# Kernel tuning notes

Measured on AMD Instinct MI355X. Metric: run time of the kernel, lower is better.

The kernel has to match this reference:

```python
import jax, jax.numpy as jnp
import numpy as np

B, S, D = 2, 2048, 2048
H, KV, HD = 32, 8, 64          # n_heads, n_kv_heads, head_dim
REP = H // KV                   # GQA repeat factor
NEG = -1e30                     # causal mask fill


def setup_inputs() -> dict:
    key = jax.random.key(0)
    ks = jax.random.split(key, 5)
    x = jax.random.normal(ks[0], (B, S, D), dtype=jnp.float32)
    # llama rotary frequencies: theta = 10000^{-2i/hd}
    inv_freq = 1.0 / (10000.0 ** (np.arange(0, HD, 2, dtype=np.float32) / HD))
    angles = np.outer(np.arange(S, dtype=np.float32), inv_freq)  # (S, HD/2)
    freqs_cos = jnp.asarray(np.cos(angles), dtype=jnp.float32)
    freqs_sin = jnp.asarray(np.sin(angles), dtype=jnp.float32)
    sc = 0.02
    wq = jax.random.normal(ks[1], (H * HD, D), dtype=jnp.float32) * sc
    wk = jax.random.normal(ks[2], (KV * HD, D), dtype=jnp.float32) * sc
    wv = jax.random.normal(ks[3], (KV * HD, D), dtype=jnp.float32) * sc
    wo = jax.random.normal(ks[4], (D, H * HD), dtype=jnp.float32) * sc
    return {"x": x, "freqs_cos": freqs_cos, "freqs_sin": freqs_sin,
            "wq": wq, "wk": wk, "wv": wv, "wo": wo}


def _rope(t, cos, sin):
    # t: (B, S, h, HD); even/odd lanes form (real, imag) pairs
    tr, ti = t[..., 0::2], t[..., 1::2]
    cos = cos[None, :, None, :]
    sin = sin[None, :, None, :]
    out_r = tr * cos - ti * sin
    out_i = tr * sin + ti * cos
    return jnp.stack([out_r, out_i], axis=-1).reshape(t.shape)


def reference(x, freqs_cos, freqs_sin, wq, wk, wv, wo):
    # QKV projections (torch Linear convention: y = x @ W.T)
    q = (x @ wq.T).reshape(B, S, H, HD)
    k = (x @ wk.T).reshape(B, S, KV, HD)
    v = (x @ wv.T).reshape(B, S, KV, HD)
    q = _rope(q, freqs_cos, freqs_sin)
    k = _rope(k, freqs_cos, freqs_sin)
    # GQA: group query heads instead of materializing repeat_kv
    q = q.transpose(0, 2, 1, 3).reshape(B, KV, REP, S, HD)  # (B,g,r,S,HD)
    k = k.transpose(0, 2, 1, 3)                              # (B,g,S,HD)
    v = v.transpose(0, 2, 1, 3)                              # (B,g,S,HD)
    scores = jnp.einsum('bgrqh,bgkh->bgrqk', q, k) / np.float32(np.sqrt(HD))
    causal = jnp.tril(jnp.ones((S, S), dtype=bool))
    scores = jnp.where(causal[None, None, None], scores, NEG)
    probs = jax.nn.softmax(scores, axis=-1)
    out = jnp.einsum('bgrqk,bgkh->bgrqh', probs, v)
    out = out.reshape(B, H, S, HD).transpose(0, 2, 1, 3).reshape(B, S, H * HD)
    return out @ wo.T
```

## Files before the change

kernel.cpp:

```cpp
#include <hip/hip_runtime.h>
#include <stdint.h>

#define S_LEN 2048
#define D_DIM 2048
#define NH 32
#define NKV 8
#define HD 64
#define B_SZ 2
#define QKV_N 3072
#define K_OFF 2048
#define V_OFF 2560
#define SCL 0.1803368801111244f

typedef unsigned short ushort_t;
typedef __attribute__((ext_vector_type(8))) short short8;
typedef __attribute__((ext_vector_type(4))) float f32x4;
typedef __attribute__((ext_vector_type(16))) float f32x16;

__device__ __forceinline__ float b2f(ushort_t u) {
  union { unsigned int i; float f; } x; x.i = ((unsigned int)u) << 16; return x.f;
}
__device__ __forceinline__ ushort_t f2b(float f) {
  union { float f; unsigned int i; } x; x.f = f;
  unsigned int r = x.i + 0x7FFFu + ((x.i >> 16) & 1u);
  return (ushort_t)(r >> 16);
}

__device__ __forceinline__ void load_lds16(const ushort_t* g, ushort_t* l) {
  __builtin_amdgcn_global_load_lds(
      (const __attribute__((address_space(1))) void*)g,
      (__attribute__((address_space(3))) void*)l, 16, 0, 0);
}

__device__ __forceinline__ short8 ld_swz(const ushort_t* base, int row, int colElem) {
  int byte = (row << 7) + (colElem << 1);
  byte ^= (row & 7) << 4;
  return *(const short8*)((const char*)base + byte);
}

__device__ __forceinline__ uint32_t cvtpk(float a, float b) {
  uint32_t r;
  asm("v_cvt_pk_bf16_f32 %0, %1, %2" : "=v"(r) : "v"(a), "v"(b));
  return r;
}
__device__ __forceinline__ void pswap(uint32_t& a, uint32_t& b) {
  asm("v_permlane32_swap_b32 %0, %1" : "+v"(a), "+v"(b));
}
__device__ __forceinline__ short8 mk8(uint32_t w0, uint32_t w1, uint32_t w2, uint32_t w3) {
  union { uint32_t w[4]; short8 v; } u;
  u.w[0] = w0; u.w[1] = w1; u.w[2] = w2; u.w[3] = w3;
  return u.v;
}

__global__ void cvt_bf16(const float* __restrict__ in, ushort_t* __restrict__ out, int n8) {
  int i = blockIdx.x * blockDim.x + threadIdx.x;
  if (i >= n8) return;
  const float4* p = (const float4*)(in + (size_t)i * 8);
  float4 x0 = p[0], x1 = p[1];
  ushort_t u[8] = { f2b(x0.x), f2b(x0.y), f2b(x0.z), f2b(x0.w),
                    f2b(x1.x), f2b(x1.y), f2b(x1.z), f2b(x1.w) };
  *(uint4*)(out + (size_t)i * 8) = *(const uint4*)u;
}

template <int HEADS, int LOG2H>
__global__ void rope_kernel(ushort_t* __restrict__ t, const float* __restrict__ cosT,
                            const float* __restrict__ sinT, int n8) {
  int idx = blockIdx.x * blockDim.x + threadIdx.x;
  if (idx >= n8) return;
  int d8 = idx & 7;
  int rest = idx >> 3;
  int h = rest & (HEADS - 1);
  int row = rest >> LOG2H;
  int s = row & (S_LEN - 1);
  float4 c4 = *(const float4*)(cosT + s * 32 + d8 * 4);
  float4 s4 = *(const float4*)(sinT + s * 32 + d8 * 4);
  ushort_t* p = t + (size_t)row * QKV_N + h * HD + d8 * 8;
  ushort_t u[8]; *(uint4*)u = *(const uint4*)p;
  float c[4] = { c4.x, c4.y, c4.z, c4.w }, sn[4] = { s4.x, s4.y, s4.z, s4.w };
  ushort_t o[8];
#pragma unroll
  for (int j = 0; j < 4; ++j) {
    float re = b2f(u[2 * j]), im = b2f(u[2 * j + 1]);
    o[2 * j]     = f2b(re * c[j] - im * sn[j]);
    o[2 * j + 1] = f2b(re * sn[j] + im * c[j]);
  }
  *(uint4*)p = *(const uint4*)o;
}

__global__ __launch_bounds__(256) void transpose_v(const ushort_t* __restrict__ v,
                                                   ushort_t* __restrict__ vt) {
  __shared__ ushort_t tile[64][80];
  int st = blockIdx.x, g = blockIdx.y, b = blockIdx.z;
  int tid = threadIdx.x;
#pragma unroll
  for (int p = 0; p < 2; ++p) {
    int o = p * 2048 + tid * 8;
    int s = o >> 6, d = o & 63;
    uint4 val = *(const uint4*)(v + ((size_t)(b * S_LEN + st * 64 + s) * QKV_N + g * HD + d));
    *(uint4*)&tile[s][d] = val;
  }
  __syncthreads();
#pragma unroll
  for (int p = 0; p < 2; ++p) {
    int o = p * 2048 + tid * 8;
    int d = o >> 6, s0 = o & 63;
    ushort_t tmp[8];
#pragma unroll
    for (int j = 0; j < 8; ++j) tmp[j] = tile[s0 + j][d];
    *(uint4*)(vt + (((size_t)(b * NKV + g) * HD + d) * S_LEN + st * 64 + s0)) = *(const uint4*)tmp;
  }
}

template <typename OutT>
__global__ __launch_bounds__(256) void gemm_bt(const ushort_t* __restrict__ A,
                                               const ushort_t* __restrict__ Bw,
                                               OutT* __restrict__ C,
                                               int M, int N, int K) {
  __shared__ ushort_t As[128 * 32];
  __shared__ ushort_t Bs[128 * 32];
  const int tid = threadIdx.x;
  const int lane = tid & 63, wave = tid >> 6;
  const int wr = wave >> 1, wc = wave & 1;
  const size_t rb = (size_t)blockIdx.y * 128;
  const size_t cb = (size_t)blockIdx.x * 128;
  f32x4 acc[4][4];
#pragma unroll
  for (int i = 0; i < 4; ++i)
#pragma unroll
    for (int j = 0; j < 4; ++j) acc[i][j] = (f32x4){0.f, 0.f, 0.f, 0.f};

  for (int k0 = 0; k0 < K; k0 += 32) {
    __syncthreads();
#pragma unroll
    for (int c = 0; c < 2; ++c) {
      const int o = c * 4096 + wave * 1024 + lane * 16;
      const int r = o >> 6;
      const int col = (o >> 1) & 31;
      load_lds16(A + (rb + r) * K + k0 + col, As + (c * 4096 + wave * 1024) / 2);
      load_lds16(Bw + (cb + r) * K + k0 + col, Bs + (c * 4096 + wave * 1024) / 2);
    }
    __syncthreads();
    short8 a[4], b[4];
#pragma unroll
    for (int i = 0; i < 4; ++i) {
      a[i] = *(const short8*)(As + (wr * 64 + i * 16 + (lane & 15)) * 32 + (lane >> 4) * 8);
      b[i] = *(const short8*)(Bs + (wc * 64 + i * 16 + (lane & 15)) * 32 + (lane >> 4) * 8);
    }
#pragma unroll
    for (int i = 0; i < 4; ++i)
#pragma unroll
      for (int j = 0; j < 4; ++j)
        acc[i][j] = __builtin_amdgcn_mfma_f32_16x16x32_bf16(a[i], b[j], acc[i][j], 0, 0, 0);
  }
#pragma unroll
  for (int i = 0; i < 4; ++i) {
    const size_t r0 = rb + wr * 64 + i * 16 + ((lane >> 4) * 4);
#pragma unroll
    for (int j = 0; j < 4; ++j) {
      const size_t c0 = cb + wc * 64 + j * 16 + (lane & 15);
#pragma unroll
      for (int r = 0; r < 4; ++r) {
        float v = acc[i][j][r];
        if constexpr (sizeof(OutT) == 2) C[(r0 + r) * N + c0] = f2b(v);
        else                             C[(r0 + r) * N + c0] = v;
      }
    }
  }
}

__global__ __launch_bounds__(256) void flash_attn(const ushort_t* __restrict__ q,
                                                  const ushort_t* __restrict__ k,
                                                  const ushort_t* __restrict__ vt,
                                                  ushort_t* __restrict__ out) {
  __shared__ ushort_t Ks[2][64 * 64];
  __shared__ ushort_t Vs[2][64 * 64];
  const int pairIdx = blockIdx.x, h = blockIdx.y, b = blockIdx.z;
  const int g = h >> 2;
  const int tid = threadIdx.x, lane = tid & 63, wave = tid >> 6;
  const int l31 = lane & 31, hi = lane >> 5;

  int srcRow[2], srcCol[2], ldsOff[2];
#pragma unroll
  for (int c = 0; c < 2; ++c) {
    const int o = c * 4096 + wave * 1024 + lane * 16;
    const int r = o >> 7;
    srcRow[c] = r;
    srcCol[c] = ((o & 127) ^ ((r & 7) << 4)) >> 1;
    ldsOff[c] = (c * 4096 + wave * 1024) / 2;
  }
  const ushort_t* kbase = k + (size_t)b * S_LEN * QKV_N + g * HD;
  const ushort_t* vbase = vt + (size_t)(b * NKV + g) * HD * S_LEN;

#pragma unroll 1
  for (int halfi = 0; halfi < 2; ++halfi) {
    const int qt = (halfi == 0) ? pairIdx : (15 - pairIdx);
    const int q0 = qt * 128;
    const int qwbase = q0 + wave * 32;
    const int qglob = qwbase + l31;

    short8 qf[4];
    {
      const ushort_t* qp = q + (size_t)(b * S_LEN + qglob) * QKV_N + h * HD + hi * 8;
#pragma unroll
      for (int s = 0; s < 4; ++s) qf[s] = *(const short8*)(qp + s * 16);
    }
    f32x16 oacc[2];
#pragma unroll
    for (int d = 0; d < 2; ++d)
#pragma unroll
      for (int r = 0; r < 16; ++r) oacc[d][r] = 0.f;
    float msc = -3e38f, lrow = 0.f;

#pragma unroll
    for (int c = 0; c < 2; ++c) {
      load_lds16(kbase + (size_t)srcRow[c] * QKV_N + srcCol[c], &Ks[0][ldsOff[c]]);
      load_lds16(vbase + (size_t)srcRow[c] * S_LEN + srcCol[c], &Vs[0][ldsOff[c]]);
    }
    __syncthreads();

    int cur = 0;
    const int nt = 2 * (qt + 1);
    for (int t = 0; t < nt; ++t) {
      const int kv0 = t * 64;
      if (t + 1 < nt) {
        const int nk = kv0 + 64;
#pragma unroll
        for (int c = 0; c < 2; ++c) {
          load_lds16(kbase + (size_t)(nk + srcRow[c]) * QKV_N + srcCol[c], &Ks[cur ^ 1][ldsOff[c]]);
          load_lds16(vbase + (size_t)srcRow[c] * S_LEN + nk + srcCol[c], &Vs[cur ^ 1][ldsOff[c]]);
        }
      }
      if (kv0 <= qwbase + 31) {
        f32x16 pacc[2];
#pragma unroll
        for (int j = 0; j < 2; ++j) {
          f32x16 z;
#pragma unroll
          for (int r = 0; r < 16; ++r) z[r] = 0.f;
#pragma unroll
          for (int s = 0; s < 4; ++s) {
            short8 kf = ld_swz(Ks[cur], j * 32 + l31, s * 16 + hi * 8);
            z = __builtin_amdgcn_mfma_f32_32x32x16_bf16(kf, qf[s], z, 0, 0, 0);
          }
          pacc[j] = z;
        }
        if (kv0 + 63 > qwbase) {
#pragma unroll
          for (int j = 0; j < 2; ++j)
#pragma unroll
            for (int r = 0; r < 16; ++r) {
              const int kvabs = kv0 + j * 32 + (r & 3) + 8 * (r >> 2) + 4 * hi;
              pacc[j][r] = (kvabs <= qglob) ? pacc[j][r] : -1e30f;
            }
        }
        float mraw = -3e38f;
#pragma unroll
        for (int j = 0; j < 2; ++j)
#pragma unroll
          for (int r = 0; r < 16; ++r) mraw = fmaxf(mraw, pacc[j][r]);
        mraw = fmaxf(mraw, __shfl_xor(mraw, 32));
        const float mscn = fmaxf(msc, mraw * SCL);
        const float sold = exp2f(msc - mscn);
        msc = mscn;
        float rs = 0.f;
        short8 pf[4];
#pragma unroll
        for (int j = 0; j < 2; ++j) {
          float pv[16];
#pragma unroll
          for (int r = 0; r < 16; ++r) {
            pv[r] = exp2f(pacc[j][r] * SCL - msc);
            rs += pv[r];
          }
          uint32_t w0 = cvtpk(pv[0], pv[1]),  w1 = cvtpk(pv[2], pv[3]);
          uint32_t w2 = cvtpk(pv[4], pv[5]),  w3 = cvtpk(pv[6], pv[7]);
          uint32_t w4 = cvtpk(pv[8], pv[9]),  w5 = cvtpk(pv[10], pv[11]);
          uint32_t w6 = cvtpk(pv[12], pv[13]), w7 = cvtpk(pv[14], pv[15]);
          pswap(w0, w2); pswap(w1, w3); pswap(w4, w6); pswap(w5, w7);
          pf[2 * j]     = mk8(w0, w1, w2, w3);
          pf[2 * j + 1] = mk8(w4, w5, w6, w7);
        }
        rs += __shfl_xor(rs, 32);
        lrow = lrow * sold + rs;
#pragma unroll
        for (int dblk = 0; dblk < 2; ++dblk) {
#pragma unroll
          for (int r = 0; r < 16; ++r) oacc[dblk][r] *= sold;
#pragma unroll
          for (int s = 0; s < 4; ++s) {
            short8 vf = ld_swz(Vs[cur], dblk * 32 + l31, s * 16 + hi * 8);
            oacc[dblk] = __builtin_amdgcn_mfma_f32_32x32x16_bf16(vf, pf[s], oacc[dblk], 0, 0, 0);
          }
        }
      }
      __syncthreads();
      cur ^= 1;
    }
    const float inv = 1.f / lrow;
    ushort_t* op = out + (size_t)(b * S_LEN + qglob) * (NH * HD) + h * HD;
#pragma unroll
    for (int dblk = 0; dblk < 2; ++dblk) {
      float ov[16];
#pragma unroll
      for (int r = 0; r < 16; ++r) ov[r] = oacc[dblk][r] * inv;
      uint32_t w0 = cvtpk(ov[0], ov[1]),  w1 = cvtpk(ov[2], ov[3]);
      uint32_t w2 = cvtpk(ov[4], ov[5]),  w3 = cvtpk(ov[6], ov[7]);
      uint32_t w4 = cvtpk(ov[8], ov[9]),  w5 = cvtpk(ov[10], ov[11]);
      uint32_t w6 = cvtpk(ov[12], ov[13]), w7 = cvtpk(ov[14], ov[15]);
      pswap(w0, w2); pswap(w1, w3); pswap(w4, w6); pswap(w5, w7);
      uint4 stlo; stlo.x = w0; stlo.y = w1; stlo.z = w2; stlo.w = w3;
      uint4 sthi; sthi.x = w4; sthi.y = w5; sthi.z = w6; sthi.w = w7;
      *(uint4*)(op + dblk * 32 + hi * 8)      = stlo;
      *(uint4*)(op + dblk * 32 + 16 + hi * 8) = sthi;
    }
  }
}

extern "C" void kernel_launch(void* const* d_in, const int* in_sizes, int n_in,
                              void* d_out, int out_size, void* d_ws, size_t ws_size,
                              hipStream_t stream) {
  const float* x  = (const float*)d_in[0];
  const float* fc = (const float*)d_in[1];
  const float* fs = (const float*)d_in[2];
  const float* wq = (const float*)d_in[3];
  const float* wk = (const float*)d_in[4];
  const float* wv = (const float*)d_in[5];
  const float* wo = (const float*)d_in[6];
  float* out = (float*)d_out;
  ushort_t* ws = (ushort_t*)d_ws;

  const size_t n_x   = (size_t)B_SZ * S_LEN * D_DIM;
  const size_t n_wq  = (size_t)NH * HD * D_DIM;
  const size_t n_wk  = (size_t)NKV * HD * D_DIM;
  const size_t n_qkv = (size_t)B_SZ * S_LEN * QKV_N;
  const size_t n_q   = (size_t)B_SZ * S_LEN * NH * HD;
  const size_t n_k   = (size_t)B_SZ * S_LEN * NKV * HD;

  size_t off = 0;
  ushort_t* xb   = ws + off; off += n_x;
  ushort_t* wqb  = ws + off; off += n_wq;
  ushort_t* wkb  = ws + off; off += n_wk;
  ushort_t* wvb  = ws + off; off += n_wk;
  ushort_t* wob  = ws + off; off += n_wq;
  ushort_t* qkvb = ws + off; off += n_qkv;
  ushort_t* vtb  = ws + off; off += n_k;
  ushort_t* ab   = ws + off; off += n_q;
  (void)ws_size; (void)in_sizes; (void)n_in; (void)out_size;

  auto cvt = [&](const float* src, ushort_t* dst, size_t n) {
    int n8 = (int)(n / 8);
    cvt_bf16<<<dim3((n8 + 255) / 256), dim3(256), 0, stream>>>(src, dst, n8);
  };
  cvt(x, xb, n_x);
  cvt(wq, wqb, n_wq);
  cvt(wk, wkb, n_wk);
  cvt(wv, wvb, n_wk);
  cvt(wo, wob, n_wq);

  const int M = B_SZ * S_LEN;
  gemm_bt<ushort_t><<<dim3(QKV_N / 128, M / 128), 256, 0, stream>>>(xb, wqb, qkvb, M, QKV_N, D_DIM);

  rope_kernel<NH, 5><<<dim3((M * NH * 8) / 256), 256, 0, stream>>>(qkvb, fc, fs, M * NH * 8);
  rope_kernel<NKV, 3><<<dim3((M * NKV * 8) / 256), 256, 0, stream>>>(qkvb + K_OFF, fc, fs, M * NKV * 8);

  transpose_v<<<dim3(S_LEN / 64, NKV, B_SZ), 256, 0, stream>>>(qkvb + V_OFF, vtb);

  flash_attn<<<dim3(8, NH, B_SZ), 256, 0, stream>>>(qkvb, qkvb + K_OFF, vtb, ab);

  gemm_bt<float><<<dim3(D_DIM / 128, M / 128), 256, 0, stream>>>(ab, wob, out, M, D_DIM, D_DIM);
}
```

Measured before the change: 244.3 us.

## Split flash-attention pairs into heaviest-first blocks, lazy rescale, XCD remap GEMM

Flash attention no longer pairs a light and a heavy query tile per block. It launches one block per query tile, ordered heaviest first, doubling the grid for better load balance across CUs. It also adds s_setprio around the MFMA sections and skips the running-max rescale unless the max grows by more than 8 (log2 units), which avoids exp and multiply work but lets unnormalised values grow. The GEMM block index is remapped so neighbouring tiles land on the same XCD, to improve L2 reuse.

```diff
diff --git a/kernel.cpp b/kernel.cpp
--- a/kernel.cpp
+++ b/kernel.cpp
@@ -121,8 +121,11 @@
   const int tid = threadIdx.x;
   const int lane = tid & 63, wave = tid >> 6;
   const int wr = wave >> 1, wc = wave & 1;
-  const size_t rb = (size_t)blockIdx.y * 128;
-  const size_t cb = (size_t)blockIdx.x * 128;
+  const int nwg = gridDim.x * gridDim.y;
+  const int orig = blockIdx.y * gridDim.x + blockIdx.x;
+  const int w = ((orig & 7) * (nwg >> 3)) + (orig >> 3);
+  const size_t rb = (size_t)(w / gridDim.x) * 128;
+  const size_t cb = (size_t)(w % gridDim.x) * 128;
   f32x4 acc[4][4];
 #pragma unroll
   for (int i = 0; i < 4; ++i)
@@ -174,7 +177,8 @@
                                                   ushort_t* __restrict__ out) {
   __shared__ ushort_t Ks[2][64 * 64];
   __shared__ ushort_t Vs[2][64 * 64];
-  const int pairIdx = blockIdx.x, h = blockIdx.y, b = blockIdx.z;
+  const int qt = 15 - blockIdx.x;
+  const int h = blockIdx.y, b = blockIdx.z;
   const int g = h >> 2;
   const int tid = threadIdx.x, lane = tid & 63, wave = tid >> 6;
   const int l31 = lane & 31, hi = lane >> 5;
@@ -191,128 +195,133 @@
   const ushort_t* kbase = k + (size_t)b * S_LEN * QKV_N + g * HD;
   const ushort_t* vbase = vt + (size_t)(b * NKV + g) * HD * S_LEN;
 
-#pragma unroll 1
-  for (int halfi = 0; halfi < 2; ++halfi) {
-    const int qt = (halfi == 0) ? pairIdx : (15 - pairIdx);
-    const int q0 = qt * 128;
-    const int qwbase = q0 + wave * 32;
-    const int qglob = qwbase + l31;
-
-    short8 qf[4];
-    {
-      const ushort_t* qp = q + (size_t)(b * S_LEN + qglob) * QKV_N + h * HD + hi * 8;
-#pragma unroll
-      for (int s = 0; s < 4; ++s) qf[s] = *(const short8*)(qp + s * 16);
-    }
-    f32x16 oacc[2];
-#pragma unroll
-    for (int d = 0; d < 2; ++d)
-#pragma unroll
-      for (int r = 0; r < 16; ++r) oacc[d][r] = 0.f;
-    float msc = -3e38f, lrow = 0.f;
-
-#pragma unroll
-    for (int c = 0; c < 2; ++c) {
-      load_lds16(kbase + (size_t)srcRow[c] * QKV_N + srcCol[c], &Ks[0][ldsOff[c]]);
-      load_lds16(vbase + (size_t)srcRow[c] * S_LEN + srcCol[c], &Vs[0][ldsOff[c]]);
+  const int qwbase = qt * 128 + wave * 32;
+  const int qglob = qwbase + l31;
+
+  short8 qf[4];
+  {
+    const ushort_t* qp = q + (size_t)(b * S_LEN + qglob) * QKV_N + h * HD + hi * 8;
+#pragma unroll
+    for (int s = 0; s < 4; ++s) qf[s] = *(const short8*)(qp + s * 16);
+  }
+  f32x16 oacc[2];
+#pragma unroll
+  for (int d = 0; d < 2; ++d)
+#pragma unroll
+    for (int r = 0; r < 16; ++r) oacc[d][r] = 0.f;
+  float msc = -3e38f, lrow = 0.f;
+
+#pragma unroll
+  for (int c = 0; c < 2; ++c) {
+    load_lds16(kbase + (size_t)srcRow[c] * QKV_N + srcCol[c], &Ks[0][ldsOff[c]]);
+    load_lds16(vbase + (size_t)srcRow[c] * S_LEN + srcCol[c], &Vs[0][ldsOff[c]]);
+  }
+  __syncthreads();
+
+  int cur = 0;
+  const int nt = 2 * (qt + 1);
+  for (int t = 0; t < nt; ++t) {
+    const int kv0 = t * 64;
+    if (t + 1 < nt) {
+      const int nk = kv0 + 64;
+#pragma unroll
+      for (int c = 0; c < 2; ++c) {
+        load_lds16(kbase + (size_t)(nk + srcRow[c]) * QKV_N + srcCol[c], &Ks[cur ^ 1][ldsOff[c]]);
+        load_lds16(vbase + (size_t)srcRow[c] * S_LEN + nk + srcCol[c], &Vs[cur ^ 1][ldsOff[c]]);
+      }
+    }
+    if (kv0 <= qwbase + 31) {
+      f32x16 pacc[2];
+      __builtin_amdgcn_s_setprio(1);
+#pragma unroll
+      for (int j = 0; j < 2; ++j) {
+        f32x16 z;
+#pragma unroll
+        for (int r = 0; r < 16; ++r) z[r] = 0.f;
+#pragma unroll
+        for (int s = 0; s < 4; ++s) {
+          short8 kf = ld_swz(Ks[cur], j * 32 + l31, s * 16 + hi * 8);
+          z = __builtin_amdgcn_mfma_f32_32x32x16_bf16(kf, qf[s], z, 0, 0, 0);
+        }
+        pacc[j] = z;
+      }
+      __builtin_amdgcn_s_setprio(0);
+      if (kv0 + 63 > qwbase) {
+#pragma unroll
+        for (int j = 0; j < 2; ++j)
+#pragma unroll
+          for (int r = 0; r < 16; ++r) {
+            const int kvabs = kv0 + j * 32 + (r & 3) + 8 * (r >> 2) + 4 * hi;
+            pacc[j][r] = (kvabs <= qglob) ? pacc[j][r] : -1e30f;
+          }
+      }
+      float mraw = -3e38f;
+#pragma unroll
+      for (int j = 0; j < 2; ++j)
+#pragma unroll
+        for (int r = 0; r < 16; ++r) mraw = fmaxf(mraw, pacc[j][r]);
+      mraw = fmaxf(mraw, __shfl_xor(mraw, 32));
+      const float mscaled = mraw * SCL;
+      if (__any(mscaled - msc > 8.f)) {
+        const float mnew = fmaxf(msc, mscaled);
+        const float sold = exp2f(msc - mnew);
+        msc = mnew;
+        lrow *= sold;
+#pragma unroll
+        for (int dblk = 0; dblk < 2; ++dblk)
+#pragma unroll
+          for (int r = 0; r < 16; ++r) oacc[dblk][r] *= sold;
+      }
+      float rs = 0.f;
+      short8 pf[4];
+#pragma unroll
+      for (int j = 0; j < 2; ++j) {
+        float pv[16];
+#pragma unroll
+        for (int r = 0; r < 16; ++r) {
+          pv[r] = exp2f(pacc[j][r] * SCL - msc);
+          rs += pv[r];
+        }
+        uint32_t w0 = cvtpk(pv[0], pv[1]),  w1 = cvtpk(pv[2], pv[3]);
+        uint32_t w2 = cvtpk(pv[4], pv[5]),  w3 = cvtpk(pv[6], pv[7]);
+        uint32_t w4 = cvtpk(pv[8], pv[9]),  w5 = cvtpk(pv[10], pv[11]);
+        uint32_t w6 = cvtpk(pv[12], pv[13]), w7 = cvtpk(pv[14], pv[15]);
+        pswap(w0, w2); pswap(w1, w3); pswap(w4, w6); pswap(w5, w7);
+        pf[2 * j]     = mk8(w0, w1, w2, w3);
+        pf[2 * j + 1] = mk8(w4, w5, w6, w7);
+      }
+      rs += __shfl_xor(rs, 32);
+      lrow += rs;
+      __builtin_amdgcn_s_setprio(1);
+#pragma unroll
+      for (int dblk = 0; dblk < 2; ++dblk) {
+#pragma unroll
+        for (int s = 0; s < 4; ++s) {
+          short8 vf = ld_swz(Vs[cur], dblk * 32 + l31, s * 16 + hi * 8);
+          oacc[dblk] = __builtin_amdgcn_mfma_f32_32x32x16_bf16(vf, pf[s], oacc[dblk], 0, 0, 0);
+        }
+      }
+      __builtin_amdgcn_s_setprio(0);
     }
     __syncthreads();
-
-    int cur = 0;
-    const int nt = 2 * (qt + 1);
-    for (int t = 0; t < nt; ++t) {
-      const int kv0 = t * 64;
-      if (t + 1 < nt) {
-        const int nk = kv0 + 64;
-#pragma unroll
-        for (int c = 0; c < 2; ++c) {
-          load_lds16(kbase + (size_t)(nk + srcRow[c]) * QKV_N + srcCol[c], &Ks[cur ^ 1][ldsOff[c]]);
-          load_lds16(vbase + (size_t)srcRow[c] * S_LEN + nk + srcCol[c], &Vs[cur ^ 1][ldsOff[c]]);
-        }
-      }
-      if (kv0 <= qwbase + 31) {
-        f32x16 pacc[2];
-#pragma unroll
-        for (int j = 0; j < 2; ++j) {
-          f32x16 z;
-#pragma unroll
-          for (int r = 0; r < 16; ++r) z[r] = 0.f;
-#pragma unroll
-          for (int s = 0; s < 4; ++s) {
-            short8 kf = ld_swz(Ks[cur], j * 32 + l31, s * 16 + hi * 8);
-            z = __builtin_amdgcn_mfma_f32_32x32x16_bf16(kf, qf[s], z, 0, 0, 0);
-          }
-          pacc[j] = z;
-        }
-        if (kv0 + 63 > qwbase) {
-#pragma unroll
-          for (int j = 0; j < 2; ++j)
-#pragma unroll
-            for (int r = 0; r < 16; ++r) {
-              const int kvabs = kv0 + j * 32 + (r & 3) + 8 * (r >> 2) + 4 * hi;
-              pacc[j][r] = (kvabs <= qglob) ? pacc[j][r] : -1e30f;
-            }
-        }
-        float mraw = -3e38f;
-#pragma unroll
-        for (int j = 0; j < 2; ++j)
-#pragma unroll
-          for (int r = 0; r < 16; ++r) mraw = fmaxf(mraw, pacc[j][r]);
-        mraw = fmaxf(mraw, __shfl_xor(mraw, 32));
-        const float mscn = fmaxf(msc, mraw * SCL);
-        const float sold = exp2f(msc - mscn);
-        msc = mscn;
-        float rs = 0.f;
-        short8 pf[4];
-#pragma unroll
-        for (int j = 0; j < 2; ++j) {
-          float pv[16];
-#pragma unroll
-          for (int r = 0; r < 16; ++r) {
-            pv[r] = exp2f(pacc[j][r] * SCL - msc);
-            rs += pv[r];
-          }
-          uint32_t w0 = cvtpk(pv[0], pv[1]),  w1 = cvtpk(pv[2], pv[3]);
-          uint32_t w2 = cvtpk(pv[4], pv[5]),  w3 = cvtpk(pv[6], pv[7]);
-          uint32_t w4 = cvtpk(pv[8], pv[9]),  w5 = cvtpk(pv[10], pv[11]);
-          uint32_t w6 = cvtpk(pv[12], pv[13]), w7 = cvtpk(pv[14], pv[15]);
-          pswap(w0, w2); pswap(w1, w3); pswap(w4, w6); pswap(w5, w7);
-          pf[2 * j]     = mk8(w0, w1, w2, w3);
-          pf[2 * j + 1] = mk8(w4, w5, w6, w7);
-        }
-        rs += __shfl_xor(rs, 32);
-        lrow = lrow * sold + rs;
-#pragma unroll
-        for (int dblk = 0; dblk < 2; ++dblk) {
-#pragma unroll
-          for (int r = 0; r < 16; ++r) oacc[dblk][r] *= sold;
-#pragma unroll
-          for (int s = 0; s < 4; ++s) {
-            short8 vf = ld_swz(Vs[cur], dblk * 32 + l31, s * 16 + hi * 8);
-            oacc[dblk] = __builtin_amdgcn_mfma_f32_32x32x16_bf16(vf, pf[s], oacc[dblk], 0, 0, 0);
-          }
-        }
-      }
-      __syncthreads();
-      cur ^= 1;
-    }
-    const float inv = 1.f / lrow;
-    ushort_t* op = out + (size_t)(b * S_LEN + qglob) * (NH * HD) + h * HD;
-#pragma unroll
-    for (int dblk = 0; dblk < 2; ++dblk) {
-      float ov[16];
-#pragma unroll
-      for (int r = 0; r < 16; ++r) ov[r] = oacc[dblk][r] * inv;
-      uint32_t w0 = cvtpk(ov[0], ov[1]),  w1 = cvtpk(ov[2], ov[3]);
-      uint32_t w2 = cvtpk(ov[4], ov[5]),  w3 = cvtpk(ov[6], ov[7]);
-      uint32_t w4 = cvtpk(ov[8], ov[9]),  w5 = cvtpk(ov[10], ov[11]);
-      uint32_t w6 = cvtpk(ov[12], ov[13]), w7 = cvtpk(ov[14], ov[15]);
-      pswap(w0, w2); pswap(w1, w3); pswap(w4, w6); pswap(w5, w7);
-      uint4 stlo; stlo.x = w0; stlo.y = w1; stlo.z = w2; stlo.w = w3;
-      uint4 sthi; sthi.x = w4; sthi.y = w5; sthi.z = w6; sthi.w = w7;
-      *(uint4*)(op + dblk * 32 + hi * 8)      = stlo;
-      *(uint4*)(op + dblk * 32 + 16 + hi * 8) = sthi;
-    }
+    cur ^= 1;
+  }
+  const float inv = 1.f / lrow;
+  ushort_t* op = out + (size_t)(b * S_LEN + qglob) * (NH * HD) + h * HD;
+#pragma unroll
+  for (int dblk = 0; dblk < 2; ++dblk) {
+    float ov[16];
+#pragma unroll
+    for (int r = 0; r < 16; ++r) ov[r] = oacc[dblk][r] * inv;
+    uint32_t w0 = cvtpk(ov[0], ov[1]),  w1 = cvtpk(ov[2], ov[3]);
+    uint32_t w2 = cvtpk(ov[4], ov[5]),  w3 = cvtpk(ov[6], ov[7]);
+    uint32_t w4 = cvtpk(ov[8], ov[9]),  w5 = cvtpk(ov[10], ov[11]);
+    uint32_t w6 = cvtpk(ov[12], ov[13]), w7 = cvtpk(ov[14], ov[15]);
+    pswap(w0, w2); pswap(w1, w3); pswap(w4, w6); pswap(w5, w7);
+    uint4 stlo; stlo.x = w0; stlo.y = w1; stlo.z = w2; stlo.w = w3;
+    uint4 sthi; sthi.x = w4; sthi.y = w5; sthi.z = w6; sthi.w = w7;
+    *(uint4*)(op + dblk * 32 + hi * 8)      = stlo;
+    *(uint4*)(op + dblk * 32 + 16 + hi * 8) = sthi;
   }
 }
 
@@ -365,7 +374,7 @@
 
   transpose_v<<<dim3(S_LEN / 64, NKV, B_SZ), 256, 0, stream>>>(qkvb + V_OFF, vtb);
 
-  flash_attn<<<dim3(8, NH, B_SZ), 256, 0, stream>>>(qkvb, qkvb + K_OFF, vtb, ab);
+  flash_attn<<<dim3(16, NH, B_SZ), 256, 0, stream>>>(qkvb, qkvb + K_OFF, vtb, ab);
 
   gemm_bt<float><<<dim3(D_DIM / 128, M / 128), 256, 0, stream>>>(ab, wob, out, M, D_DIM, D_DIM);
 }
```

After: 291.6 us. 19.4% more time.

## Replace GEMM with 256x256 8-wave double-buffered pipelined kernel

Applied to the files above, without the earlier changes.

Replaces the simple 128x128 single-buffered GEMM, which had two barriers per 32-wide k step, with a 256x256 tile, 512-thread kernel. The new kernel stages 64-wide k slices into double-buffered, XOR-swizzled LDS via direct global-to-LDS loads and interleaves partial loads with MFMA quarters. It also adds explicit vmcnt waits, s_setprio around the MFMA blocks and a workgroup remapping for L2 locality. The aim is to hide global load latency and increase data reuse per tile. In exchange it uses much more LDS (128 KB per block), has fewer blocks in flight, and relies on hand-tuned wait counts for correctness.

```diff
diff --git a/kernel.cpp b/kernel.cpp
--- a/kernel.cpp
+++ b/kernel.cpp
@@ -16,6 +16,10 @@
 typedef __attribute__((ext_vector_type(8))) short short8;
 typedef __attribute__((ext_vector_type(4))) float f32x4;
 typedef __attribute__((ext_vector_type(16))) float f32x16;
+
+#define SBAR() do { __builtin_amdgcn_sched_barrier(0); __builtin_amdgcn_s_barrier(); __builtin_amdgcn_sched_barrier(0); } while (0)
+#define WAITV4() asm volatile("s_waitcnt vmcnt(4)" ::: "memory")
+#define WAITV0() asm volatile("s_waitcnt vmcnt(0)" ::: "memory")
 
 __device__ __forceinline__ float b2f(ushort_t u) {
   union { unsigned int i; float f; } x; x.i = ((unsigned int)u) << 16; return x.f;
@@ -111,56 +115,101 @@
   }
 }
 
+#define DSR(MH, NH) \
+  _Pragma("unroll") for (int mi = 0; mi < 4; ++mi) \
+    _Pragma("unroll") for (int ks = 0; ks < 2; ++ks) \
+      af[mi][ks] = ld_swz(Ac, wr * 128 + ((MH) * 4 + mi) * 16 + l15, ks * 32 + lhi * 8); \
+  _Pragma("unroll") for (int ni = 0; ni < 2; ++ni) \
+    _Pragma("unroll") for (int ks = 0; ks < 2; ++ks) \
+      bfr[ni][ks] = ld_swz(Bc, wc * 64 + ((NH) * 2 + ni) * 16 + l15, ks * 32 + lhi * 8);
+
+#define MFM(MH, NH) \
+  _Pragma("unroll") for (int mi = 0; mi < 4; ++mi) \
+    _Pragma("unroll") for (int ni = 0; ni < 2; ++ni) \
+      _Pragma("unroll") for (int ks = 0; ks < 2; ++ks) \
+        acc[(MH) * 4 + mi][(NH) * 2 + ni] = __builtin_amdgcn_mfma_f32_16x16x32_bf16( \
+            af[mi][ks], bfr[ni][ks], acc[(MH) * 4 + mi][(NH) * 2 + ni], 0, 0, 0);
+
 template <typename OutT>
-__global__ __launch_bounds__(256) void gemm_bt(const ushort_t* __restrict__ A,
-                                               const ushort_t* __restrict__ Bw,
-                                               OutT* __restrict__ C,
-                                               int M, int N, int K) {
-  __shared__ ushort_t As[128 * 32];
-  __shared__ ushort_t Bs[128 * 32];
-  const int tid = threadIdx.x;
-  const int lane = tid & 63, wave = tid >> 6;
-  const int wr = wave >> 1, wc = wave & 1;
-  const size_t rb = (size_t)blockIdx.y * 128;
-  const size_t cb = (size_t)blockIdx.x * 128;
-  f32x4 acc[4][4];
-#pragma unroll
-  for (int i = 0; i < 4; ++i)
+__global__ __launch_bounds__(512, 2) void gemm8_bt(const ushort_t* __restrict__ A,
+                                                   const ushort_t* __restrict__ Bw,
+                                                   OutT* __restrict__ C,
+                                                   int M, int N, int K) {
+  __shared__ ushort_t Ab[2][256 * 64];
+  __shared__ ushort_t Bb[2][256 * 64];
+  const int tid = threadIdx.x, lane = tid & 63, wave = tid >> 6;
+  const int wr = wave >> 2, wc = wave & 3;
+  const int l15 = lane & 15, lhi = lane >> 4;
+  const int nwg = gridDim.x * gridDim.y;
+  const int orig = blockIdx.y * gridDim.x + blockIdx.x;
+  const int w = ((orig & 7) * (nwg >> 3)) + (orig >> 3);
+  const size_t rb = (size_t)(w / gridDim.x) * 256;
+  const size_t cb = (size_t)(w % gridDim.x) * 256;
+  const int NK = K >> 6;
+
+  auto stageA = [&](int kt, ushort_t* dst, int g) {
+#pragma unroll
+    for (int p = 0; p < 2; ++p) {
+      const int ub = p * 16384 + g * 8192 + wave * 1024;
+      const int lb = ub + lane * 16;
+      const int row = lb >> 7;
+      const int csw = ((lb & 127) ^ ((row & 7) << 4)) >> 1;
+      load_lds16(A + (rb + row) * (size_t)K + kt * 64 + csw,
+                 (ushort_t*)((char*)dst + ub));
+    }
+  };
+  auto stageB = [&](int kt, ushort_t* dst, int g) {
+#pragma unroll
+    for (int p = 0; p < 2; ++p) {
+      const int ub = p * 16384 + (wave >> 2) * 8192 + g * 4096 + (wave & 3) * 1024;
+      const int lb = ub + lane * 16;
+      const int row = lb >> 7;
+      const int csw = ((lb & 127) ^ ((row & 7) << 4)) >> 1;
+      load_lds16(Bw + (cb + row) * (size_t)K + kt * 64 + csw,
+                 (ushort_t*)((char*)dst + ub));
+    }
+  };
+
+  f32x4 acc[8][4];
+#pragma unroll
+  for (int i = 0; i < 8; ++i)
 #pragma unroll
     for (int j = 0; j < 4; ++j) acc[i][j] = (f32x4){0.f, 0.f, 0.f, 0.f};
 
-  for (int k0 = 0; k0 < K; k0 += 32) {
-    __syncthreads();
-#pragma unroll
-    for (int c = 0; c < 2; ++c) {
-      const int o = c * 4096 + wave * 1024 + lane * 16;
-      const int r = o >> 6;
-      const int col = (o >> 1) & 31;
-      load_lds16(A + (rb + r) * K + k0 + col, As + (c * 4096 + wave * 1024) / 2);
-      load_lds16(Bw + (cb + r) * K + k0 + col, Bs + (c * 4096 + wave * 1024) / 2);
-    }
-    __syncthreads();
-    short8 a[4], b[4];
-#pragma unroll
-    for (int i = 0; i < 4; ++i) {
-      a[i] = *(const short8*)(As + (wr * 64 + i * 16 + (lane & 15)) * 32 + (lane >> 4) * 8);
-      b[i] = *(const short8*)(Bs + (wc * 64 + i * 16 + (lane & 15)) * 32 + (lane >> 4) * 8);
-    }
-#pragma unroll
-    for (int i = 0; i < 4; ++i)
-#pragma unroll
-      for (int j = 0; j < 4; ++j)
-        acc[i][j] = __builtin_amdgcn_mfma_f32_16x16x32_bf16(a[i], b[j], acc[i][j], 0, 0, 0);
-  }
-#pragma unroll
-  for (int i = 0; i < 4; ++i) {
-    const size_t r0 = rb + wr * 64 + i * 16 + ((lane >> 4) * 4);
-#pragma unroll
-    for (int j = 0; j < 4; ++j) {
-      const size_t c0 = cb + wc * 64 + j * 16 + (lane & 15);
+  stageA(0, Ab[0], 0); stageA(0, Ab[0], 1);
+  stageB(0, Bb[0], 0); stageB(0, Bb[0], 1);
+  stageA(1, Ab[1], 0); stageB(1, Bb[1], 0);
+  WAITV4();
+  SBAR();
+
+  short8 af[4][2], bfr[2][2];
+#pragma unroll 1
+  for (int kt = 0; kt < NK; ++kt) {
+    ushort_t* Ac = Ab[kt & 1];
+    ushort_t* Bc = Bb[kt & 1];
+    ushort_t* An = Ab[(kt & 1) ^ 1];
+    ushort_t* Bn = Bb[(kt & 1) ^ 1];
+    DSR(0, 0); if (kt + 1 < NK) stageA(kt + 1, An, 1);
+    SBAR(); __builtin_amdgcn_s_setprio(1); MFM(0, 0); __builtin_amdgcn_s_setprio(0); SBAR();
+    DSR(0, 1); if (kt + 1 < NK) stageB(kt + 1, Bn, 1);
+    SBAR(); __builtin_amdgcn_s_setprio(1); MFM(0, 1); __builtin_amdgcn_s_setprio(0); SBAR();
+    DSR(1, 0); if (kt + 2 < NK) stageA(kt + 2, Ac, 0);
+    SBAR(); __builtin_amdgcn_s_setprio(1); MFM(1, 0); __builtin_amdgcn_s_setprio(0); SBAR();
+    DSR(1, 1); if (kt + 2 < NK) stageB(kt + 2, Bc, 0);
+    SBAR(); __builtin_amdgcn_s_setprio(1); MFM(1, 1); __builtin_amdgcn_s_setprio(0);
+    if (kt + 2 < NK) { WAITV4(); } else if (kt + 1 < NK) { WAITV0(); }
+    SBAR();
+  }
+
+#pragma unroll
+  for (int m = 0; m < 8; ++m) {
+    const size_t r0 = rb + wr * 128 + m * 16 + lhi * 4;
+#pragma unroll
+    for (int n = 0; n < 4; ++n) {
+      const size_t c0 = cb + wc * 64 + n * 16 + l15;
 #pragma unroll
       for (int r = 0; r < 4; ++r) {
-        float v = acc[i][j][r];
+        float v = acc[m][n][r];
         if constexpr (sizeof(OutT) == 2) C[(r0 + r) * N + c0] = f2b(v);
         else                             C[(r0 + r) * N + c0] = v;
       }
@@ -194,8 +243,7 @@
 #pragma unroll 1
   for (int halfi = 0; halfi < 2; ++halfi) {
     const int qt = (halfi == 0) ? pairIdx : (15 - pairIdx);
-    const int q0 = qt * 128;
-    const int qwbase = q0 + wave * 32;
+    const int qwbase = qt * 128 + wave * 32;
     const int qglob = qwbase + l31;
 
     short8 qf[4];
@@ -358,7 +406,7 @@
   cvt(wo, wob, n_wq);
 
   const int M = B_SZ * S_LEN;
-  gemm_bt<ushort_t><<<dim3(QKV_N / 128, M / 128), 256, 0, stream>>>(xb, wqb, qkvb, M, QKV_N, D_DIM);
+  gemm8_bt<ushort_t><<<dim3(QKV_N / 256, M / 256), 512, 0, stream>>>(xb, wqb, qkvb, M, QKV_N, D_DIM);
 
   rope_kernel<NH, 5><<<dim3((M * NH * 8) / 256), 256, 0, stream>>>(qkvb, fc, fs, M * NH * 8);
   rope_kernel<NKV, 3><<<dim3((M * NKV * 8) / 256), 256, 0, stream>>>(qkvb + K_OFF, fc, fs, M * NKV * 8);
@@ -367,5 +415,5 @@
 
   flash_attn<<<dim3(8, NH, B_SZ), 256, 0, stream>>>(qkvb, qkvb + K_OFF, vtb, ab);
 
-  gemm_bt<float><<<dim3(D_DIM / 128, M / 128), 256, 0, stream>>>(ab, wob, out, M, D_DIM, D_DIM);
-}
+  gemm8_bt<float><<<dim3(D_DIM / 256, M / 256), 512, 0, stream>>>(ab, wob, out, M, D_DIM, D_DIM);
+}
```

After: 261.0 us. +6.8%, slower.

## Split flash attention KV range in two with merge kernel; swizzle GEMM block order

Applied to the files above, without the earlier changes.

Flash attention now splits each query tile's causal KV range into two halves handled by separate workgroups. Each half writes an unnormalized bf16 partial output plus its running max and sum, and a new merge kernel combines them. The grid doubles to 1024 workgroups to raise occupancy on the many-CU GPU. The cost is extra global traffic for the partials, an extra launch, and an added bf16 rounding of unnormalized partials. The GEMM also remaps block indices in an XCD-aware interleaved order to improve cache locality.

```diff
diff --git a/kernel.cpp b/kernel.cpp
--- a/kernel.cpp
+++ b/kernel.cpp
@@ -121,8 +121,11 @@
   const int tid = threadIdx.x;
   const int lane = tid & 63, wave = tid >> 6;
   const int wr = wave >> 1, wc = wave & 1;
-  const size_t rb = (size_t)blockIdx.y * 128;
-  const size_t cb = (size_t)blockIdx.x * 128;
+  const int nwg = gridDim.x * gridDim.y;
+  const int orig = blockIdx.y * gridDim.x + blockIdx.x;
+  const int w = ((orig & 7) * (nwg >> 3)) + (orig >> 3);
+  const size_t rb = (size_t)(w / gridDim.x) * 128;
+  const size_t cb = (size_t)(w % gridDim.x) * 128;
   f32x4 acc[4][4];
 #pragma unroll
   for (int i = 0; i < 4; ++i)
@@ -171,10 +174,12 @@
 __global__ __launch_bounds__(256) void flash_attn(const ushort_t* __restrict__ q,
                                                   const ushort_t* __restrict__ k,
                                                   const ushort_t* __restrict__ vt,
-                                                  ushort_t* __restrict__ out) {
+                                                  ushort_t* __restrict__ pO,
+                                                  float2* __restrict__ pml) {
   __shared__ ushort_t Ks[2][64 * 64];
   __shared__ ushort_t Vs[2][64 * 64];
-  const int pairIdx = blockIdx.x, h = blockIdx.y, b = blockIdx.z;
+  const int pairIdx = blockIdx.x >> 1, split = blockIdx.x & 1;
+  const int h = blockIdx.y, b = blockIdx.z;
   const int g = h >> 2;
   const int tid = threadIdx.x, lane = tid & 63, wave = tid >> 6;
   const int l31 = lane & 31, hi = lane >> 5;
@@ -194,9 +199,9 @@
 #pragma unroll 1
   for (int halfi = 0; halfi < 2; ++halfi) {
     const int qt = (halfi == 0) ? pairIdx : (15 - pairIdx);
-    const int q0 = qt * 128;
-    const int qwbase = q0 + wave * 32;
+    const int qwbase = qt * 128 + wave * 32;
     const int qglob = qwbase + l31;
+    const int t0 = split * (qt + 1), t1 = t0 + (qt + 1);
 
     short8 qf[4];
     {
@@ -213,16 +218,15 @@
 
 #pragma unroll
     for (int c = 0; c < 2; ++c) {
-      load_lds16(kbase + (size_t)srcRow[c] * QKV_N + srcCol[c], &Ks[0][ldsOff[c]]);
-      load_lds16(vbase + (size_t)srcRow[c] * S_LEN + srcCol[c], &Vs[0][ldsOff[c]]);
+      load_lds16(kbase + (size_t)(t0 * 64 + srcRow[c]) * QKV_N + srcCol[c], &Ks[0][ldsOff[c]]);
+      load_lds16(vbase + (size_t)srcRow[c] * S_LEN + t0 * 64 + srcCol[c], &Vs[0][ldsOff[c]]);
     }
     __syncthreads();
 
     int cur = 0;
-    const int nt = 2 * (qt + 1);
-    for (int t = 0; t < nt; ++t) {
+    for (int t = t0; t < t1; ++t) {
       const int kv0 = t * 64;
-      if (t + 1 < nt) {
+      if (t + 1 < t1) {
         const int nk = kv0 + 64;
 #pragma unroll
         for (int c = 0; c < 2; ++c) {
@@ -296,13 +300,14 @@
       __syncthreads();
       cur ^= 1;
     }
-    const float inv = 1.f / lrow;
-    ushort_t* op = out + (size_t)(b * S_LEN + qglob) * (NH * HD) + h * HD;
+    const int pidx = ((b * S_LEN + qglob) * NH + h) * 2 + split;
+    pml[pidx] = make_float2(msc, lrow);
+    ushort_t* op = pO + (size_t)pidx * 64;
 #pragma unroll
     for (int dblk = 0; dblk < 2; ++dblk) {
       float ov[16];
 #pragma unroll
-      for (int r = 0; r < 16; ++r) ov[r] = oacc[dblk][r] * inv;
+      for (int r = 0; r < 16; ++r) ov[r] = oacc[dblk][r];
       uint32_t w0 = cvtpk(ov[0], ov[1]),  w1 = cvtpk(ov[2], ov[3]);
       uint32_t w2 = cvtpk(ov[4], ov[5]),  w3 = cvtpk(ov[6], ov[7]);
       uint32_t w4 = cvtpk(ov[8], ov[9]),  w5 = cvtpk(ov[10], ov[11]);
@@ -314,6 +319,25 @@
       *(uint4*)(op + dblk * 32 + 16 + hi * 8) = sthi;
     }
   }
+}
+
+__global__ void merge_split(const ushort_t* __restrict__ pO, const float2* __restrict__ pml,
+                            ushort_t* __restrict__ ab, int n) {
+  int gid = blockIdx.x * blockDim.x + threadIdx.x;
+  if (gid >= n) return;
+  const int r = gid >> 3, d8 = gid & 7;
+  const float2 ml1 = pml[r * 2], ml2 = pml[r * 2 + 1];
+  const float mm = fmaxf(ml1.x, ml2.x);
+  const float s1 = exp2f(ml1.x - mm), s2 = exp2f(ml2.x - mm);
+  const float inv = 1.f / (ml1.y * s1 + ml2.y * s2);
+  uint4 a = *(const uint4*)(pO + ((size_t)r * 2) * 64 + d8 * 8);
+  uint4 c = *(const uint4*)(pO + ((size_t)r * 2 + 1) * 64 + d8 * 8);
+  ushort_t ua[8], uc[8], o[8];
+  *(uint4*)ua = a; *(uint4*)uc = c;
+#pragma unroll
+  for (int j = 0; j < 8; ++j)
+    o[j] = f2b((b2f(ua[j]) * s1 + b2f(uc[j]) * s2) * inv);
+  *(uint4*)(ab + (size_t)r * 64 + d8 * 8) = *(const uint4*)o;
 }
 
 extern "C" void kernel_launch(void* const* d_in, const int* in_sizes, int n_in,
@@ -335,6 +359,7 @@
   const size_t n_qkv = (size_t)B_SZ * S_LEN * QKV_N;
   const size_t n_q   = (size_t)B_SZ * S_LEN * NH * HD;
   const size_t n_k   = (size_t)B_SZ * S_LEN * NKV * HD;
+  const size_t n_rows = (size_t)B_SZ * S_LEN * NH;
 
   size_t off = 0;
   ushort_t* xb   = ws + off; off += n_x;
@@ -345,6 +370,8 @@
   ushort_t* qkvb = ws + off; off += n_qkv;
   ushort_t* vtb  = ws + off; off += n_k;
   ushort_t* ab   = ws + off; off += n_q;
+  ushort_t* pO   = ws + off; off += n_rows * 2 * 64;
+  float2*   pml  = (float2*)(ws + off); off += n_rows * 2 * 2;
   (void)ws_size; (void)in_sizes; (void)n_in; (void)out_size;
 
   auto cvt = [&](const float* src, ushort_t* dst, size_t n) {
@@ -365,7 +392,10 @@
 
   transpose_v<<<dim3(S_LEN / 64, NKV, B_SZ), 256, 0, stream>>>(qkvb + V_OFF, vtb);
 
-  flash_attn<<<dim3(8, NH, B_SZ), 256, 0, stream>>>(qkvb, qkvb + K_OFF, vtb, ab);
+  flash_attn<<<dim3(16, NH, B_SZ), 256, 0, stream>>>(qkvb, qkvb + K_OFF, vtb, pO, pml);
+
+  const int nmerge = (int)(n_rows * 8);
+  merge_split<<<dim3(nmerge / 256), 256, 0, stream>>>(pO, pml, ab, nmerge);
 
   gemm_bt<float><<<dim3(D_DIM / 128, M / 128), 256, 0, stream>>>(ab, wob, out, M, D_DIM, D_DIM);
 }
```

After: 252.6 us. +3.4%, slower.
